# Performance work log

Hardware: AMD Instinct MI355X
Metric: run time of the kernel (lower is better)

## Reference

```python
import jax, jax.numpy as jnp
import numpy as np

NUM_HEADS = 16

def setup_inputs() -> dict:
    key = jax.random.key(0)
    k1, k2, k3 = jax.random.split(key, 3)
    B, N, C = 4, 4096, 1024
    x = jax.random.normal(k1, (B, N, C), dtype=jnp.float32)
    y = jax.random.normal(k2, (B, N, C), dtype=jnp.float32)
    # nn.Linear(embed_dim, embed_dim): weight [C, C], bias [C]
    W_proj = jax.random.normal(k3, (C, C), dtype=jnp.float32) * (1.0 / np.sqrt(C))
    b_proj = jnp.zeros((C,), dtype=jnp.float32)
    return {"x": x, "y": y, "W_proj": W_proj, "b_proj": b_proj}

def reference(x, y, W_proj, b_proj):
    B, N, C = x.shape
    H = NUM_HEADS
    d = C // H
    # NOTE: no head transpose in the original -> scores are over the HEAD axis.
    q = x.reshape(B, N, H, d)
    k = y.reshape(B, N, H, d)
    v = y.reshape(B, N, H, d)
    # attn: [B, N, H, H], per-token head-to-head scores
    attn = jnp.einsum('bnhd,bngd->bnhg', q, k) / jnp.sqrt(jnp.asarray(d, x.dtype))
    attn = jax.nn.softmax(attn, axis=-1)
    # dropout(p=0.1) is identity in eval mode
    o = jnp.einsum('bnhg,bngd->bnhd', attn, v)          # [B, N, H, d]
    # x.transpose(1, 2).reshape(B, N, C) in torch:
    o = jnp.transpose(o, (0, 2, 1, 3)).reshape(B, N, C)
    out = o @ W_proj.T + b_proj
    return out
```

## Files before the change

### kernel.cpp

```cpp
#include <hip/hip_runtime.h>
#include <hip/hip_bf16.h>
#include <stdint.h>

typedef __attribute__((ext_vector_type(8))) short bf16x8;
typedef __attribute__((ext_vector_type(4))) short bf16x4;
typedef __attribute__((ext_vector_type(4))) float f32x4;
typedef __attribute__((ext_vector_type(4))) int   i32x4;

static __device__ __forceinline__ short f2bs(float f) {
  __hip_bfloat16 h = __float2bfloat16(f);
  return __builtin_bit_cast(short, h);
}

__device__ __forceinline__ void gload_lds16(const void* g, void* l) {
  auto* gp = reinterpret_cast<__attribute__((address_space(1))) uint32_t*>((uintptr_t)g);
  auto* lp = reinterpret_cast<__attribute__((address_space(3))) uint32_t*>((uintptr_t)l);
  __builtin_amdgcn_global_load_lds(gp, lp, 16, 0, 0);
}

__global__ __launch_bounds__(256) void attn_kernel(
    const float* __restrict__ x, const float* __restrict__ y,
    __hip_bfloat16* __restrict__ A,
    const float* __restrict__ W, __hip_bfloat16* __restrict__ Wb)
{
  if (blockIdx.x < 1024) {
    const int i = (blockIdx.x * 256 + threadIdx.x) * 4;
    const float4 v = *(const float4*)(W + i);
    Wb[i + 0] = __float2bfloat16(v.x);
    Wb[i + 1] = __float2bfloat16(v.y);
    Wb[i + 2] = __float2bfloat16(v.z);
    Wb[i + 3] = __float2bfloat16(v.w);
  }

  const int wid  = threadIdx.x >> 6;
  const int lane = threadIdx.x & 63;
  const int tok  = blockIdx.x * 4 + wid;
  const int b    = tok >> 12;
  const int n    = tok & 4095;

  const float* xr = x + (size_t)tok * 1024;
  const float* yr = y + (size_t)tok * 1024;

  const int c  = lane & 15;
  const int qq = lane >> 4;

  const int fbase = c * 64 + qq * 8;
  bf16x8 yf[2], xf[2];
  #pragma unroll
  for (int kk = 0; kk < 2; ++kk) {
    const float4 a0 = *(const float4*)(yr + fbase + kk * 32);
    const float4 a1 = *(const float4*)(yr + fbase + kk * 32 + 4);
    const float4 b0 = *(const float4*)(xr + fbase + kk * 32);
    const float4 b1 = *(const float4*)(xr + fbase + kk * 32 + 4);
    yf[kk] = bf16x8{f2bs(a0.x), f2bs(a0.y), f2bs(a0.z), f2bs(a0.w),
                    f2bs(a1.x), f2bs(a1.y), f2bs(a1.z), f2bs(a1.w)};
    xf[kk] = bf16x8{f2bs(b0.x), f2bs(b0.y), f2bs(b0.z), f2bs(b0.w),
                    f2bs(b1.x), f2bs(b1.y), f2bs(b1.z), f2bs(b1.w)};
  }

  f32x4 acc = {0.f, 0.f, 0.f, 0.f};
  acc = __builtin_amdgcn_mfma_f32_16x16x32_bf16(yf[0], xf[0], acc, 0, 0, 0);
  acc = __builtin_amdgcn_mfma_f32_16x16x32_bf16(yf[1], xf[1], acc, 0, 0, 0);

  float sc[4];
  #pragma unroll
  for (int r = 0; r < 4; ++r) sc[r] = acc[r] * 0.125f;
  float mx = fmaxf(fmaxf(sc[0], sc[1]), fmaxf(sc[2], sc[3]));
  mx = fmaxf(mx, __shfl_xor(mx, 16));
  mx = fmaxf(mx, __shfl_xor(mx, 32));
  float e[4];
  #pragma unroll
  for (int r = 0; r < 4; ++r) e[r] = __expf(sc[r] - mx);
  float sm = (e[0] + e[1]) + (e[2] + e[3]);
  sm += __shfl_xor(sm, 16);
  sm += __shfl_xor(sm, 32);
  const float inv = 1.0f / sm;
  float p[4];
  #pragma unroll
  for (int r = 0; r < 4; ++r) p[r] = e[r] * inv;

  f32x4 o[4];
  #pragma unroll
  for (int q = 0; q < 4; ++q) o[q] = f32x4{0.f, 0.f, 0.f, 0.f};

#if __has_builtin(__builtin_amdgcn_mfma_f32_16x16x16bf16_1k)
  const bf16x4 pa = {f2bs(p[0]), f2bs(p[1]), f2bs(p[2]), f2bs(p[3])};
  #pragma unroll
  for (int q = 0; q < 4; ++q) {
    bf16x4 bq;
    #pragma unroll
    for (int j = 0; j < 4; ++j)
      bq[j] = f2bs(yr[(qq * 4 + j) * 64 + q * 16 + c]);
    o[q] = __builtin_amdgcn_mfma_f32_16x16x16bf16_1k(pa, bq, o[q], 0, 0, 0);
  }
#else
  const int u0 = ((int)(unsigned short)f2bs(p[1]) << 16) | (unsigned short)f2bs(p[0]);
  const int u1 = ((int)(unsigned short)f2bs(p[3]) << 16) | (unsigned short)f2bs(p[2]);
  const int s0 = c + 32 * qq;
  int a0 = __shfl(u0, s0), a1 = __shfl(u1, s0);
  int a2 = __shfl(u0, s0 + 16), a3 = __shfl(u1, s0 + 16);
  const bool valid = (qq < 2);
  if (!valid) { a0 = 0; a1 = 0; a2 = 0; a3 = 0; }
  const bf16x8 a8 = __builtin_bit_cast(bf16x8, i32x4{a0, a1, a2, a3});
  #pragma unroll
  for (int q = 0; q < 4; ++q) {
    bf16x8 b8;
    #pragma unroll
    for (int j = 0; j < 8; ++j) {
      const int g = (qq * 8 + j) & 15;
      const float v = yr[g * 64 + q * 16 + c];
      b8[j] = valid ? f2bs(v) : (short)0;
    }
    o[q] = __builtin_amdgcn_mfma_f32_16x16x32_bf16(a8, b8, o[q], 0, 0, 0);
  }
#endif

  const size_t base = ((size_t)b * 4096 + (n >> 4)) * 1024 + ((n & 15) << 6) + c;
  #pragma unroll
  for (int q = 0; q < 4; ++q)
    #pragma unroll
    for (int r = 0; r < 4; ++r) {
      const int h = qq * 4 + r;
      A[base + (size_t)h * 262144 + q * 16] = __float2bfloat16(o[q][r]);
    }
}

#define FENCE asm volatile("" ::: "memory")
#define BAR   __builtin_amdgcn_s_barrier()
#define LGKM0 asm volatile("s_waitcnt lgkmcnt(0)" ::: "memory")
#define VM6   asm volatile("s_waitcnt vmcnt(6)" ::: "memory")
#define VM0   asm volatile("s_waitcnt vmcnt(0)" ::: "memory")
#define SB0   __builtin_amdgcn_sched_barrier(0)
#define SP1   __builtin_amdgcn_s_setprio(1)
#define SP0   __builtin_amdgcn_s_setprio(0)

__global__ __launch_bounds__(256, 2) void gemm_wt(
    const __hip_bfloat16* __restrict__ A,
    const __hip_bfloat16* __restrict__ Bw,
    const float* __restrict__ bias,
    float* __restrict__ C)
{
  __shared__ char ldsA[3 * 16384];
  __shared__ char ldsB[3 * 8192];

  const int tid  = threadIdx.x;
  const int lane = tid & 63;
  const int wid  = tid >> 6;
  const int wr   = wid >> 1;
  const int wc   = wid & 1;

  const int bid   = blockIdx.x;
  const int mg    = (bid & 7) | (((bid >> 3) & 7) << 3);
  const int nt    = (bid >> 6) & 7;
  const int mBase = mg * 256;
  const int nBase = nt * 128;

  const int srow = tid >> 2;
  const int lcb  = (((tid & 3) ^ ((srow >> 1) & 3)) << 4);
  const char* aS0 = (const char*)A  + (size_t)(mBase + srow)       * 2048 + lcb;
  const char* aS1 = (const char*)A  + (size_t)(mBase + 64 + srow)  * 2048 + lcb;
  const char* aS2 = (const char*)A  + (size_t)(mBase + 128 + srow) * 2048 + lcb;
  const char* aS3 = (const char*)A  + (size_t)(mBase + 192 + srow) * 2048 + lcb;
  const char* bS0 = (const char*)Bw + (size_t)(nBase + srow)       * 2048 + lcb;
  const char* bS1 = (const char*)Bw + (size_t)(nBase + 64 + srow)  * 2048 + lcb;

  const int fr = lane & 15;
  const int kq = lane >> 4;
  const int fq = kq;
  const int ofk  = ((kq ^ ((fr >> 1) & 3)) << 4);
  const int aOff = (wr * 128 + fr) * 64 + ofk;
  const int bOff = (wc * 64  + fr) * 64 + ofk;

  f32x4 acc[8][4];
  #pragma unroll
  for (int m = 0; m < 8; ++m)
    #pragma unroll
    for (int n = 0; n < 4; ++n) acc[m][n] = f32x4{0.f, 0.f, 0.f, 0.f};

  auto STG = [&](int sp, int buf) {
    const int ko = sp * 64;
    char* aD = ldsA + buf * 16384 + tid * 16;
    char* bD = ldsB + buf * 8192  + tid * 16;
    gload_lds16(aS0 + ko, aD);
    gload_lds16(aS1 + ko, aD + 4096);
    gload_lds16(aS2 + ko, aD + 8192);
    gload_lds16(aS3 + ko, aD + 12288);
    gload_lds16(bS0 + ko, bD);
    gload_lds16(bS1 + ko, bD + 4096);
  };

  auto STEP = [&](int s, int rb, bool stg, bool last) {
    if (last) { VM0; } else { VM6; }
    FENCE; BAR; FENCE;
    if (stg) STG(s + 2, (s + 2) % 3);
    const char* aB = ldsA + rb * 16384 + aOff;
    const char* bB = ldsB + rb * 8192  + bOff;
    bf16x8 Af[8], Bf[4];
    #pragma unroll
    for (int n = 0; n < 4; ++n) Bf[n] = *(const bf16x8*)(bB + n * 1024);
    #pragma unroll
    for (int m = 0; m < 8; ++m) Af[m] = *(const bf16x8*)(aB + m * 1024);
    LGKM0; SB0;
    SP1;
    #pragma unroll
    for (int m = 0; m < 8; ++m)
      #pragma unroll
      for (int n = 0; n < 4; ++n)
        acc[m][n] = __builtin_amdgcn_mfma_f32_16x16x32_bf16(Af[m], Bf[n], acc[m][n], 0, 0, 0);
    SP0;
  };

  STG(0, 0); STG(1, 1);

  for (int t = 0; t < 30; t += 3) {
    STEP(t,     0, true, false);
    STEP(t + 1, 1, true, false);
    STEP(t + 2, 2, true, false);
  }
  STEP(30, 0, false, false);
  STEP(31, 1, false, true);

  #pragma unroll
  for (int n = 0; n < 4; ++n) {
    const int col = nBase + wc * 64 + n * 16 + fr;
    const float bv = bias[col];
    #pragma unroll
    for (int m = 0; m < 8; ++m) {
      const int row0 = mBase + wr * 128 + m * 16 + fq * 4;
      #pragma unroll
      for (int r = 0; r < 4; ++r)
        C[(size_t)(row0 + r) * 1024 + col] = acc[m][n][r] + bv;
    }
  }
}

extern "C" void kernel_launch(void* const* d_in, const int* in_sizes, int n_in,
                              void* d_out, int out_size, void* d_ws, size_t ws_size,
                              hipStream_t stream) {
  const float* x    = (const float*)d_in[0];
  const float* y    = (const float*)d_in[1];
  const float* W    = (const float*)d_in[2];
  const float* bias = (const float*)d_in[3];
  float* out = (float*)d_out;

  __hip_bfloat16* Abuf = (__hip_bfloat16*)d_ws;
  __hip_bfloat16* Wbuf = (__hip_bfloat16*)((char*)d_ws + (size_t)16384 * 1024 * 2);

  attn_kernel<<<4096, 256, 0, stream>>>(x, y, Abuf, W, Wbuf);
  gemm_wt<<<512, 256, 0, stream>>>(Abuf, Wbuf, bias, out);
}
```

Measured before the change: 73.84 us.

## Double-buffer GEMM fragments in registers and prefetch three stages ahead

Restructures the projection GEMM main loop. It issues three global-to-LDS stages up front instead of two. It also ping-pongs two register fragment sets, so the LDS reads for the next k-step are issued before the MFMAs for the current step. This hides LDS read latency behind matrix math and gives the global loads more lead time. The cost is extra register pressure from a second A/B fragment set, plus a more intricate buffer-rotation schedule with a peeled prologue and epilogue.

```diff
diff --git a/kernel.cpp b/kernel.cpp
--- a/kernel.cpp
+++ b/kernel.cpp
@@ -128,13 +128,51 @@
 #define FENCE asm volatile("" ::: "memory")
 #define BAR   __builtin_amdgcn_s_barrier()
 #define LGKM0 asm volatile("s_waitcnt lgkmcnt(0)" ::: "memory")
+#define VM12  asm volatile("s_waitcnt vmcnt(12)" ::: "memory")
 #define VM6   asm volatile("s_waitcnt vmcnt(6)" ::: "memory")
 #define VM0   asm volatile("s_waitcnt vmcnt(0)" ::: "memory")
-#define SB0   __builtin_amdgcn_sched_barrier(0)
 #define SP1   __builtin_amdgcn_s_setprio(1)
 #define SP0   __builtin_amdgcn_s_setprio(0)
 
-__global__ __launch_bounds__(256, 2) void gemm_wt(
+#define STG(sp, wb) do {                                                  \
+    const int ko_ = (sp) * 64;                                            \
+    char* aD_ = ldsA + (wb) * 16384 + tid * 16;                           \
+    char* bD_ = ldsB + (wb) * 8192  + tid * 16;                           \
+    gload_lds16(aS0 + ko_, aD_);                                          \
+    gload_lds16(aS1 + ko_, aD_ + 4096);                                   \
+    gload_lds16(aS2 + ko_, aD_ + 8192);                                   \
+    gload_lds16(aS3 + ko_, aD_ + 12288);                                  \
+    gload_lds16(bS0 + ko_, bD_);                                          \
+    gload_lds16(bS1 + ko_, bD_ + 4096);                                   \
+  } while (0)
+
+#define RD(RA, RB_, rb) do {                                              \
+    _Pragma("unroll")                                                     \
+    for (int mf = 0; mf < 8; ++mf)                                        \
+      RA[mf] = *(const bf16x8*)(ldsA + (rb) * 16384 + aOff + mf * 1024);  \
+    _Pragma("unroll")                                                     \
+    for (int nf = 0; nf < 4; ++nf)                                        \
+      RB_[nf] = *(const bf16x8*)(ldsB + (rb) * 8192 + bOff + nf * 1024);  \
+  } while (0)
+
+#define MM(MA, MB_) do {                                                  \
+    SP1;                                                                  \
+    _Pragma("unroll")                                                     \
+    for (int m = 0; m < 8; ++m)                                           \
+      _Pragma("unroll")                                                   \
+      for (int n = 0; n < 4; ++n)                                         \
+        acc[m][n] = __builtin_amdgcn_mfma_f32_16x16x32_bf16(MA[m], MB_[n], acc[m][n], 0, 0, 0); \
+    SP0;                                                                  \
+  } while (0)
+
+#define BODY(S, RBUF, WBUF, RDA, RDB, MMA, MMB, GATE, DOSTG) do {         \
+    GATE; LGKM0; FENCE; BAR; FENCE;                                       \
+    if (DOSTG) STG((S) + 3, WBUF);                                        \
+    RD(RDA, RDB, RBUF);                                                   \
+    MM(MMA, MMB);                                                         \
+  } while (0)
+
+__global__ __launch_bounds__(256, 2) void gemm_pipe(
     const __hip_bfloat16* __restrict__ A,
     const __hip_bfloat16* __restrict__ Bw,
     const float* __restrict__ bias,
@@ -147,7 +185,7 @@
   const int lane = tid & 63;
   const int wid  = tid >> 6;
   const int wr   = wid >> 1;
-  const int wc   = wid & 1;
+  const int wcN  = wid & 1;
 
   const int bid   = blockIdx.x;
   const int mg    = (bid & 7) | (((bid >> 3) & 7) << 3);
@@ -166,10 +204,9 @@
 
   const int fr = lane & 15;
   const int kq = lane >> 4;
-  const int fq = kq;
   const int ofk  = ((kq ^ ((fr >> 1) & 3)) << 4);
   const int aOff = (wr * 128 + fr) * 64 + ofk;
-  const int bOff = (wc * 64  + fr) * 64 + ofk;
+  const int bOff = (wcN * 64  + fr) * 64 + ofk;
 
   f32x4 acc[8][4];
   #pragma unroll
@@ -177,56 +214,31 @@
     #pragma unroll
     for (int n = 0; n < 4; ++n) acc[m][n] = f32x4{0.f, 0.f, 0.f, 0.f};
 
-  auto STG = [&](int sp, int buf) {
-    const int ko = sp * 64;
-    char* aD = ldsA + buf * 16384 + tid * 16;
-    char* bD = ldsB + buf * 8192  + tid * 16;
-    gload_lds16(aS0 + ko, aD);
-    gload_lds16(aS1 + ko, aD + 4096);
-    gload_lds16(aS2 + ko, aD + 8192);
-    gload_lds16(aS3 + ko, aD + 12288);
-    gload_lds16(bS0 + ko, bD);
-    gload_lds16(bS1 + ko, bD + 4096);
-  };
-
-  auto STEP = [&](int s, int rb, bool stg, bool last) {
-    if (last) { VM0; } else { VM6; }
-    FENCE; BAR; FENCE;
-    if (stg) STG(s + 2, (s + 2) % 3);
-    const char* aB = ldsA + rb * 16384 + aOff;
-    const char* bB = ldsB + rb * 8192  + bOff;
-    bf16x8 Af[8], Bf[4];
-    #pragma unroll
-    for (int n = 0; n < 4; ++n) Bf[n] = *(const bf16x8*)(bB + n * 1024);
-    #pragma unroll
-    for (int m = 0; m < 8; ++m) Af[m] = *(const bf16x8*)(aB + m * 1024);
-    LGKM0; SB0;
-    SP1;
-    #pragma unroll
-    for (int m = 0; m < 8; ++m)
-      #pragma unroll
-      for (int n = 0; n < 4; ++n)
-        acc[m][n] = __builtin_amdgcn_mfma_f32_16x16x32_bf16(Af[m], Bf[n], acc[m][n], 0, 0, 0);
-    SP0;
-  };
-
-  STG(0, 0); STG(1, 1);
-
-  for (int t = 0; t < 30; t += 3) {
-    STEP(t,     0, true, false);
-    STEP(t + 1, 1, true, false);
-    STEP(t + 2, 2, true, false);
-  }
-  STEP(30, 0, false, false);
-  STEP(31, 1, false, true);
+  bf16x8 A0[8], B0[4], A1[8], B1[4];
+
+  STG(0, 0); STG(1, 1); STG(2, 2);
+  VM12; FENCE; BAR; FENCE;
+  RD(A0, B0, 0);
+
+  for (int g = 0; g < 5; ++g) {
+    const int s = g * 6;
+    BODY(s + 0, 1, 0, A1, B1, A0, B0, VM6, true);
+    BODY(s + 1, 2, 1, A0, B0, A1, B1, VM6, true);
+    BODY(s + 2, 0, 2, A1, B1, A0, B0, VM6, true);
+    BODY(s + 3, 1, 0, A0, B0, A1, B1, VM6, true);
+    BODY(s + 4, 2, 1, A1, B1, A0, B0, VM6, true);
+    BODY(s + 5, 0, 2, A0, B0, A1, B1, VM6, g < 4);
+  }
+  BODY(30, 1, 0, A1, B1, A0, B0, VM0, false);
+  MM(A1, B1);
 
   #pragma unroll
   for (int n = 0; n < 4; ++n) {
-    const int col = nBase + wc * 64 + n * 16 + fr;
+    const int col = nBase + wcN * 64 + n * 16 + fr;
     const float bv = bias[col];
     #pragma unroll
     for (int m = 0; m < 8; ++m) {
-      const int row0 = mBase + wr * 128 + m * 16 + fq * 4;
+      const int row0 = mBase + wr * 128 + m * 16 + kq * 4;
       #pragma unroll
       for (int r = 0; r < 4; ++r)
         C[(size_t)(row0 + r) * 1024 + col] = acc[m][n][r] + bv;
@@ -247,5 +259,5 @@
   __hip_bfloat16* Wbuf = (__hip_bfloat16*)((char*)d_ws + (size_t)16384 * 1024 * 2);
 
   attn_kernel<<<4096, 256, 0, stream>>>(x, y, Abuf, W, Wbuf);
-  gemm_wt<<<512, 256, 0, stream>>>(Abuf, Wbuf, bias, out);
-}
+  gemm_pipe<<<512, 256, 0, stream>>>(Abuf, Wbuf, bias, out);
+}
```

After: 86.05 us. 16.5% more time.

## Restructure projection GEMM into 8-wave blocks with per-wave private A pipelines

Applied to the files above, without the earlier changes.

Rewrites the output-projection GEMM to use 512-thread blocks over 512x64 output tiles. Half of the weight tile's K range (64 KB) is staged in LDS at a time. Each wave streams its own 64-row slice of A through a private double buffer, which removes the block-wide barrier from every K step. This trades the shared A/B reuse of the 256x128 tile for barrier-free per-wave pipelining. The cost is more total A/B traffic per output element and 128 KB of LDS per block, which may limit occupancy.

```diff
diff --git a/kernel.cpp b/kernel.cpp
--- a/kernel.cpp
+++ b/kernel.cpp
@@ -128,108 +128,121 @@
 #define FENCE asm volatile("" ::: "memory")
 #define BAR   __builtin_amdgcn_s_barrier()
 #define LGKM0 asm volatile("s_waitcnt lgkmcnt(0)" ::: "memory")
-#define VM6   asm volatile("s_waitcnt vmcnt(6)" ::: "memory")
+#define VM4   asm volatile("s_waitcnt vmcnt(4)" ::: "memory")
 #define VM0   asm volatile("s_waitcnt vmcnt(0)" ::: "memory")
-#define SB0   __builtin_amdgcn_sched_barrier(0)
 #define SP1   __builtin_amdgcn_s_setprio(1)
 #define SP0   __builtin_amdgcn_s_setprio(0)
 
-__global__ __launch_bounds__(256, 2) void gemm_wt(
+__global__ __launch_bounds__(512, 2) void gemm_wp(
     const __hip_bfloat16* __restrict__ A,
     const __hip_bfloat16* __restrict__ Bw,
     const float* __restrict__ bias,
     float* __restrict__ C)
 {
-  __shared__ char ldsA[3 * 16384];
-  __shared__ char ldsB[3 * 8192];
+  __shared__ char ldsB_[65536];
+  __shared__ char ldsA_[65536];
 
   const int tid  = threadIdx.x;
   const int lane = tid & 63;
   const int wid  = tid >> 6;
-  const int wr   = wid >> 1;
-  const int wc   = wid & 1;
 
   const int bid   = blockIdx.x;
-  const int mg    = (bid & 7) | (((bid >> 3) & 7) << 3);
-  const int nt    = (bid >> 6) & 7;
-  const int mBase = mg * 256;
-  const int nBase = nt * 128;
-
-  const int srow = tid >> 2;
-  const int lcb  = (((tid & 3) ^ ((srow >> 1) & 3)) << 4);
-  const char* aS0 = (const char*)A  + (size_t)(mBase + srow)       * 2048 + lcb;
-  const char* aS1 = (const char*)A  + (size_t)(mBase + 64 + srow)  * 2048 + lcb;
-  const char* aS2 = (const char*)A  + (size_t)(mBase + 128 + srow) * 2048 + lcb;
-  const char* aS3 = (const char*)A  + (size_t)(mBase + 192 + srow) * 2048 + lcb;
-  const char* bS0 = (const char*)Bw + (size_t)(nBase + srow)       * 2048 + lcb;
-  const char* bS1 = (const char*)Bw + (size_t)(nBase + 64 + srow)  * 2048 + lcb;
+  const int xcd   = bid & 7;
+  const int nt    = (bid >> 3) & 15;
+  const int mgH   = bid >> 7;
+  const int mg    = (mgH << 3) | xcd;
+  const int mBase = mg * 512;
+  const int nBase = nt * 64;
+  const int mWave = mBase + wid * 64;
+
+  const int arow = lane >> 2;
+  const char* aS0;
+  {
+    const int sl = lane & 3;
+    aS0 = (const char*)A + (size_t)(mWave + arow) * 2048
+        + ((sl ^ ((arow >> 1) & 3)) << 4);
+  }
+  char* aD = ldsA_ + wid * 8192 + lane * 16;
+
+  const char* bS;
+  {
+    const int rowb = (tid >> 2) & 63;
+    const int sl   = tid & 3;
+    bS = (const char*)Bw + (size_t)(nBase + rowb) * 2048 + ((tid >> 8) << 6)
+       + ((sl ^ ((rowb >> 1) & 3)) << 4);
+  }
 
   const int fr = lane & 15;
   const int kq = lane >> 4;
-  const int fq = kq;
-  const int ofk  = ((kq ^ ((fr >> 1) & 3)) << 4);
-  const int aOff = (wr * 128 + fr) * 64 + ofk;
-  const int bOff = (wc * 64  + fr) * 64 + ofk;
-
-  f32x4 acc[8][4];
-  #pragma unroll
-  for (int m = 0; m < 8; ++m)
+  const int rdOff = fr * 64 + ((kq ^ ((fr >> 1) & 3)) << 4);
+  const char* aRd = ldsA_ + wid * 8192 + rdOff;
+  const char* bRd = ldsB_ + rdOff;
+
+  f32x4 acc[4][4];
+  #pragma unroll
+  for (int m = 0; m < 4; ++m)
     #pragma unroll
     for (int n = 0; n < 4; ++n) acc[m][n] = f32x4{0.f, 0.f, 0.f, 0.f};
 
-  auto STG = [&](int sp, int buf) {
-    const int ko = sp * 64;
-    char* aD = ldsA + buf * 16384 + tid * 16;
-    char* bD = ldsB + buf * 8192  + tid * 16;
-    gload_lds16(aS0 + ko, aD);
-    gload_lds16(aS1 + ko, aD + 4096);
-    gload_lds16(aS2 + ko, aD + 8192);
-    gload_lds16(aS3 + ko, aD + 12288);
-    gload_lds16(bS0 + ko, bD);
-    gload_lds16(bS1 + ko, bD + 4096);
+  auto STG_A = [&](int sp) {
+    const char* s = aS0 + sp * 64;
+    char* d = aD + ((sp & 1) << 12);
+    gload_lds16(s,                       d);
+    gload_lds16(s + 16 * 2048,           d + 1024);
+    gload_lds16(s + 32 * 2048,           d + 2048);
+    gload_lds16(s + 48 * 2048,           d + 3072);
   };
 
-  auto STEP = [&](int s, int rb, bool stg, bool last) {
-    if (last) { VM0; } else { VM6; }
-    FENCE; BAR; FENCE;
-    if (stg) STG(s + 2, (s + 2) % 3);
-    const char* aB = ldsA + rb * 16384 + aOff;
-    const char* bB = ldsB + rb * 8192  + bOff;
-    bf16x8 Af[8], Bf[4];
-    #pragma unroll
-    for (int n = 0; n < 4; ++n) Bf[n] = *(const bf16x8*)(bB + n * 1024);
-    #pragma unroll
-    for (int m = 0; m < 8; ++m) Af[m] = *(const bf16x8*)(aB + m * 1024);
-    LGKM0; SB0;
+  auto BODY = [&](int s, bool stg, bool last) {
+    if (last) { VM0; } else { VM4; }
+    FENCE;
+    const int ksl = s & 15;
+    const char* aB = aRd + ((s & 1) << 12);
+    const char* bB = bRd + (ksl << 12);
+    bf16x8 Af[4], Bf[4];
+    #pragma unroll
+    for (int nf = 0; nf < 4; ++nf) Bf[nf] = *(const bf16x8*)(bB + nf * 1024);
+    #pragma unroll
+    for (int mf = 0; mf < 4; ++mf) Af[mf] = *(const bf16x8*)(aB + mf * 1024);
+    LGKM0;
+    if (stg) STG_A(s + 2);
     SP1;
     #pragma unroll
-    for (int m = 0; m < 8; ++m)
+    for (int m = 0; m < 4; ++m)
       #pragma unroll
       for (int n = 0; n < 4; ++n)
         acc[m][n] = __builtin_amdgcn_mfma_f32_16x16x32_bf16(Af[m], Bf[n], acc[m][n], 0, 0, 0);
     SP0;
   };
 
-  STG(0, 0); STG(1, 1);
-
-  for (int t = 0; t < 30; t += 3) {
-    STEP(t,     0, true, false);
-    STEP(t + 1, 1, true, false);
-    STEP(t + 2, 2, true, false);
-  }
-  STEP(30, 0, false, false);
-  STEP(31, 1, false, true);
-
-  #pragma unroll
-  for (int n = 0; n < 4; ++n) {
-    const int col = nBase + wc * 64 + n * 16 + fr;
+  #pragma unroll
+  for (int j = 0; j < 8; ++j)
+    gload_lds16(bS + j * 128, ldsB_ + j * 8192 + tid * 16);
+  STG_A(0); STG_A(1);
+  VM4; FENCE; BAR; FENCE;
+
+  for (int s = 0; s < 16; ++s) BODY(s, true, false);
+
+  FENCE; BAR; FENCE;
+  #pragma unroll
+  for (int j = 0; j < 8; ++j)
+    gload_lds16(bS + 1024 + j * 128, ldsB_ + j * 8192 + tid * 16);
+  VM4; FENCE; BAR; FENCE;
+
+  for (int s = 16; s < 30; ++s) BODY(s, true, false);
+  BODY(30, false, false);
+  BODY(31, false, true);
+
+  #pragma unroll
+  for (int nf = 0; nf < 4; ++nf) {
+    const int col = nBase + nf * 16 + fr;
     const float bv = bias[col];
     #pragma unroll
-    for (int m = 0; m < 8; ++m) {
-      const int row0 = mBase + wr * 128 + m * 16 + fq * 4;
+    for (int mf = 0; mf < 4; ++mf) {
+      const int row0 = mWave + mf * 16 + kq * 4;
       #pragma unroll
       for (int r = 0; r < 4; ++r)
-        C[(size_t)(row0 + r) * 1024 + col] = acc[m][n][r] + bv;
+        C[(size_t)(row0 + r) * 1024 + col] = acc[mf][nf][r] + bv;
     }
   }
 }
@@ -247,5 +260,5 @@
   __hip_bfloat16* Wbuf = (__hip_bfloat16*)((char*)d_ws + (size_t)16384 * 1024 * 2);
 
   attn_kernel<<<4096, 256, 0, stream>>>(x, y, Abuf, W, Wbuf);
-  gemm_wt<<<512, 256, 0, stream>>>(Abuf, Wbuf, bias, out);
-}
+  gemm_wp<<<512, 512, 0, stream>>>(Abuf, Wbuf, bias, out);
+}
```

New measurement: 81.44 us. +10.3%, slower.

## Replace pipelined 256x128 GEMM with simple single-buffered 128x128 tile kernel

Applied to the files above, without the earlier changes.

Rewrites the projection GEMM to use 128x128 output tiles with 1024 blocks instead of 256x128 tiles with 512 blocks. It drops the triple-buffered LDS pipeline, the manual waitcnt/priority scheduling and the grouped block swizzle, and uses a plain load/sync/compute/sync loop. Smaller LDS and register use allow three blocks per CU and more blocks in flight. The cost is less data reuse per tile and no overlap of global loads with MFMA work inside a block.

```diff
diff --git a/kernel.cpp b/kernel.cpp
--- a/kernel.cpp
+++ b/kernel.cpp
@@ -125,108 +125,75 @@
     }
 }
 
-#define FENCE asm volatile("" ::: "memory")
-#define BAR   __builtin_amdgcn_s_barrier()
-#define LGKM0 asm volatile("s_waitcnt lgkmcnt(0)" ::: "memory")
-#define VM6   asm volatile("s_waitcnt vmcnt(6)" ::: "memory")
-#define VM0   asm volatile("s_waitcnt vmcnt(0)" ::: "memory")
-#define SB0   __builtin_amdgcn_sched_barrier(0)
-#define SP1   __builtin_amdgcn_s_setprio(1)
-#define SP0   __builtin_amdgcn_s_setprio(0)
-
-__global__ __launch_bounds__(256, 2) void gemm_wt(
+__global__ __launch_bounds__(256, 3) void gemm_m97(
     const __hip_bfloat16* __restrict__ A,
     const __hip_bfloat16* __restrict__ Bw,
     const float* __restrict__ bias,
     float* __restrict__ C)
 {
-  __shared__ char ldsA[3 * 16384];
-  __shared__ char ldsB[3 * 8192];
+  __shared__ char ldsA[8192];
+  __shared__ char ldsB[8192];
 
   const int tid  = threadIdx.x;
   const int lane = tid & 63;
   const int wid  = tid >> 6;
   const int wr   = wid >> 1;
-  const int wc   = wid & 1;
-
-  const int bid   = blockIdx.x;
-  const int mg    = (bid & 7) | (((bid >> 3) & 7) << 3);
-  const int nt    = (bid >> 6) & 7;
-  const int mBase = mg * 256;
-  const int nBase = nt * 128;
+  const int wcN  = wid & 1;
+
+  const int bid = blockIdx.x;
+  const int nb  = (bid & 7) * 128 + (bid >> 3);
+  const int mBase = (nb >> 3) * 128;
+  const int nBase = (nb & 7) * 128;
 
   const int srow = tid >> 2;
   const int lcb  = (((tid & 3) ^ ((srow >> 1) & 3)) << 4);
-  const char* aS0 = (const char*)A  + (size_t)(mBase + srow)       * 2048 + lcb;
-  const char* aS1 = (const char*)A  + (size_t)(mBase + 64 + srow)  * 2048 + lcb;
-  const char* aS2 = (const char*)A  + (size_t)(mBase + 128 + srow) * 2048 + lcb;
-  const char* aS3 = (const char*)A  + (size_t)(mBase + 192 + srow) * 2048 + lcb;
-  const char* bS0 = (const char*)Bw + (size_t)(nBase + srow)       * 2048 + lcb;
-  const char* bS1 = (const char*)Bw + (size_t)(nBase + 64 + srow)  * 2048 + lcb;
+  const char* aS0 = (const char*)A  + (size_t)(mBase + srow)      * 2048 + lcb;
+  const char* aS1 = (const char*)A  + (size_t)(mBase + 64 + srow) * 2048 + lcb;
+  const char* bS0 = (const char*)Bw + (size_t)(nBase + srow)      * 2048 + lcb;
+  const char* bS1 = (const char*)Bw + (size_t)(nBase + 64 + srow) * 2048 + lcb;
+  char* aD = ldsA + tid * 16;
+  char* bD = ldsB + tid * 16;
 
   const int fr = lane & 15;
   const int kq = lane >> 4;
-  const int fq = kq;
   const int ofk  = ((kq ^ ((fr >> 1) & 3)) << 4);
-  const int aOff = (wr * 128 + fr) * 64 + ofk;
-  const int bOff = (wc * 64  + fr) * 64 + ofk;
-
-  f32x4 acc[8][4];
-  #pragma unroll
-  for (int m = 0; m < 8; ++m)
+  const int aOff = (wr  * 64 + fr) * 64 + ofk;
+  const int bOff = (wcN * 64 + fr) * 64 + ofk;
+
+  f32x4 acc[4][4];
+  #pragma unroll
+  for (int m = 0; m < 4; ++m)
     #pragma unroll
     for (int n = 0; n < 4; ++n) acc[m][n] = f32x4{0.f, 0.f, 0.f, 0.f};
 
-  auto STG = [&](int sp, int buf) {
-    const int ko = sp * 64;
-    char* aD = ldsA + buf * 16384 + tid * 16;
-    char* bD = ldsB + buf * 8192  + tid * 16;
+  for (int ko = 0; ko < 2048; ko += 64) {
     gload_lds16(aS0 + ko, aD);
     gload_lds16(aS1 + ko, aD + 4096);
-    gload_lds16(aS2 + ko, aD + 8192);
-    gload_lds16(aS3 + ko, aD + 12288);
     gload_lds16(bS0 + ko, bD);
     gload_lds16(bS1 + ko, bD + 4096);
-  };
-
-  auto STEP = [&](int s, int rb, bool stg, bool last) {
-    if (last) { VM0; } else { VM6; }
-    FENCE; BAR; FENCE;
-    if (stg) STG(s + 2, (s + 2) % 3);
-    const char* aB = ldsA + rb * 16384 + aOff;
-    const char* bB = ldsB + rb * 8192  + bOff;
-    bf16x8 Af[8], Bf[4];
-    #pragma unroll
-    for (int n = 0; n < 4; ++n) Bf[n] = *(const bf16x8*)(bB + n * 1024);
-    #pragma unroll
-    for (int m = 0; m < 8; ++m) Af[m] = *(const bf16x8*)(aB + m * 1024);
-    LGKM0; SB0;
-    SP1;
-    #pragma unroll
-    for (int m = 0; m < 8; ++m)
+    __syncthreads();
+
+    bf16x8 Af[4], Bf[4];
+    #pragma unroll
+    for (int n = 0; n < 4; ++n) Bf[n] = *(const bf16x8*)(ldsB + bOff + n * 1024);
+    #pragma unroll
+    for (int m = 0; m < 4; ++m) Af[m] = *(const bf16x8*)(ldsA + aOff + m * 1024);
+
+    #pragma unroll
+    for (int m = 0; m < 4; ++m)
       #pragma unroll
       for (int n = 0; n < 4; ++n)
         acc[m][n] = __builtin_amdgcn_mfma_f32_16x16x32_bf16(Af[m], Bf[n], acc[m][n], 0, 0, 0);
-    SP0;
-  };
-
-  STG(0, 0); STG(1, 1);
-
-  for (int t = 0; t < 30; t += 3) {
-    STEP(t,     0, true, false);
-    STEP(t + 1, 1, true, false);
-    STEP(t + 2, 2, true, false);
-  }
-  STEP(30, 0, false, false);
-  STEP(31, 1, false, true);
+    __syncthreads();
+  }
 
   #pragma unroll
   for (int n = 0; n < 4; ++n) {
-    const int col = nBase + wc * 64 + n * 16 + fr;
+    const int col = nBase + wcN * 64 + n * 16 + fr;
     const float bv = bias[col];
     #pragma unroll
-    for (int m = 0; m < 8; ++m) {
-      const int row0 = mBase + wr * 128 + m * 16 + fq * 4;
+    for (int m = 0; m < 4; ++m) {
+      const int row0 = mBase + wr * 64 + m * 16 + kq * 4;
       #pragma unroll
       for (int r = 0; r < 4; ++r)
         C[(size_t)(row0 + r) * 1024 + col] = acc[m][n][r] + bv;
@@ -247,5 +214,5 @@
   __hip_bfloat16* Wbuf = (__hip_bfloat16*)((char*)d_ws + (size_t)16384 * 1024 * 2);
 
   attn_kernel<<<4096, 256, 0, stream>>>(x, y, Abuf, W, Wbuf);
-  gemm_wt<<<512, 256, 0, stream>>>(Abuf, Wbuf, bias, out);
-}
+  gemm_m97<<<1024, 256, 0, stream>>>(Abuf, Wbuf, bias, out);
+}
```

Measured after the change: 76.73 us. 1.04x slower.
